# Optimization experiments

Measured on AMD Instinct MI355X. Metric: run time of the kernel, lower is better.

The kernel has to match this reference:

```python
import jax, jax.numpy as jnp
import numpy as np

B, T, D = 2, 4096, 768
H = 12
HD = D // H  # 64
SCALE = 1.0 / np.sqrt(HD)


def setup_inputs() -> dict:
    key = jax.random.key(0)
    k1, k2, k3 = jax.random.split(key, 3)
    x = jax.random.normal(k1, (B, T, D), dtype=jnp.float32)
    W_qkv = jax.random.normal(k2, (D, 3 * D), dtype=jnp.float32) * (1.0 / np.sqrt(D))
    b_qkv = jnp.zeros((3 * D,), dtype=jnp.float32)
    W_out = jax.random.normal(k3, (D, D), dtype=jnp.float32) * (1.0 / np.sqrt(D))
    b_out = jnp.zeros((D,), dtype=jnp.float32)
    return {"x": x, "W_qkv": W_qkv, "b_qkv": b_qkv, "W_out": W_out, "b_out": b_out}


def reference(x, W_qkv, b_qkv, W_out, b_out):
    Bx, Tx, C = x.shape
    qkv = x @ W_qkv + b_qkv                                  # [B,T,3D]
    qkv = qkv.reshape(Bx, Tx, 3, H, HD).transpose(2, 0, 3, 1, 4)  # [3,B,H,T,hd]
    q, k, v = qkv[0], qkv[1], qkv[2]
    scores = jnp.einsum('bhqd,bhkd->bhqk', q, k) * SCALE      # [B,H,T,T]
    causal = jnp.tril(jnp.ones((Tx, Tx), dtype=bool))
    scores = jnp.where(causal[None, None], scores, -jnp.inf)
    attn = jax.nn.softmax(scores, axis=-1)
    out = jnp.einsum('bhqk,bhkd->bhqd', attn, v)              # [B,H,T,hd]
    out = out.transpose(0, 2, 1, 3).reshape(Bx, Tx, C)        # [B,T,D]
    return out @ W_out + b_out
```

## Files before the change

kernel.cpp:

```cpp
#include <hip/hip_runtime.h>
#include <cstdint>
#include <cstddef>

typedef _Float16 f16x8 __attribute__((ext_vector_type(8)));
typedef _Float16 f16x4 __attribute__((ext_vector_type(4)));
typedef _Float16 f16x2 __attribute__((ext_vector_type(2)));
typedef float    f32x4 __attribute__((ext_vector_type(4)));

#define AS_GLOBAL __attribute__((address_space(1)))
#define AS_LDS    __attribute__((address_space(3)))

__device__ __forceinline__ void load16_to_lds(const _Float16* g, _Float16* l) {
    __builtin_amdgcn_global_load_lds((const AS_GLOBAL void*)g, (AS_LDS void*)l, 16, 0, 0);
}

#define BB   2
#define TT   4096
#define DD   768
#define NH   12
#define HDIM 64
#define D3   2304
#define SC2  (0.125f * 1.44269504088896f)

__global__ __launch_bounds__(256) void prep(const float* __restrict__ x,
                                            _Float16* __restrict__ Xh,
                                            const float* __restrict__ Wqkv,
                                            _Float16* __restrict__ Wqkvt,
                                            const float* __restrict__ Wout,
                                            _Float16* __restrict__ Wot) {
    const int bid = blockIdx.x, tid = threadIdx.x;
    if (bid < 6144) {
        const int i = bid * 1024 + tid * 4;
        float4 v = *(const float4*)(x + i);
        f16x4 h;
        h[0] = (_Float16)v.x; h[1] = (_Float16)v.y;
        h[2] = (_Float16)v.z; h[3] = (_Float16)v.w;
        *(f16x4*)(Xh + i) = h;
        return;
    }
    __shared__ float tile[32][33];
    const float* in; _Float16* out; int C, bx, by;
    if (bid < 7872) {
        const int t = bid - 6144;
        in = Wqkv; out = Wqkvt; C = 2304;
        bx = (t % 72) * 32; by = (t / 72) * 32;
    } else {
        const int t = bid - 7872;
        in = Wout; out = Wot; C = 768;
        bx = (t % 24) * 32; by = (t / 24) * 32;
    }
    const int R = 768;
    const int tx = tid & 31, ty = tid >> 5;
#pragma unroll
    for (int j = 0; j < 32; j += 8)
        tile[ty + j][tx] = in[(size_t)(by + ty + j) * C + bx + tx];
    __syncthreads();
#pragma unroll
    for (int j = 0; j < 32; j += 8)
        out[(size_t)(bx + ty + j) * R + by + tx] = (_Float16)tile[tx][ty + j];
}

template <typename OutT>
__device__ __forceinline__ void gemm_body(const _Float16* __restrict__ A,
                                          const _Float16* __restrict__ Bt,
                                          const float* __restrict__ bias, bool bias_row,
                                          OutT* __restrict__ C, int N, int K,
                                          int m0, int n0,
                                          _Float16* As, _Float16* Bs) {
    const int tid  = threadIdx.x;
    const int wave = tid >> 6, lane = tid & 63, quad = lane >> 4, l16 = lane & 15;
    const int wm = (wave & 1) * 64, wn = (wave >> 1) * 64;
    const int rowc = lane >> 3, part = lane & 7;

    f32x4 acc[4][4];
#pragma unroll
    for (int i = 0; i < 4; ++i)
#pragma unroll
        for (int n = 0; n < 4; ++n) acc[i][n] = f32x4{0.f, 0.f, 0.f, 0.f};

    for (int k0 = 0; k0 < K; k0 += 64) {
        __syncthreads();
#pragma unroll
        for (int cc = 0; cc < 4; ++cc) {
            const int ch = wave * 4 + cc;
            load16_to_lds(A  + (size_t)(m0 + ch * 8 + rowc) * K + k0 + part * 8,
                          As + ch * 512);
            load16_to_lds(Bt + (size_t)(n0 + ch * 8 + rowc) * K + k0 + part * 8,
                          Bs + ch * 512);
        }
        __syncthreads();
#pragma unroll
        for (int i = 0; i < 4; ++i) {
            f16x8 a0 = *(const f16x8*)(As + (wm + i * 16 + l16) * 64 + quad * 8);
            f16x8 a1 = *(const f16x8*)(As + (wm + i * 16 + l16) * 64 + 32 + quad * 8);
#pragma unroll
            for (int n = 0; n < 4; ++n) {
                f16x8 b0 = *(const f16x8*)(Bs + (wn + n * 16 + l16) * 64 + quad * 8);
                f16x8 b1 = *(const f16x8*)(Bs + (wn + n * 16 + l16) * 64 + 32 + quad * 8);
                acc[i][n] = __builtin_amdgcn_mfma_f32_16x16x32_f16(a0, b0, acc[i][n], 0, 0, 0);
                acc[i][n] = __builtin_amdgcn_mfma_f32_16x16x32_f16(a1, b1, acc[i][n], 0, 0, 0);
            }
        }
    }
#pragma unroll
    for (int i = 0; i < 4; ++i)
#pragma unroll
        for (int n = 0; n < 4; ++n)
#pragma unroll
            for (int r = 0; r < 4; ++r) {
                const int row = m0 + wm + i * 16 + quad * 4 + r;
                const int col = n0 + wn + n * 16 + l16;
                const float bv = bias_row ? bias[row] : bias[col];
                C[(size_t)row * N + col] = (OutT)(acc[i][n][r] + bv);
            }
}

__global__ __launch_bounds__(256) void gemm_qkv(const _Float16* __restrict__ Xh,
                                                const _Float16* __restrict__ Wqkvt,
                                                const float* __restrict__ bqkv,
                                                _Float16* __restrict__ QKh,
                                                _Float16* __restrict__ VtG) {
    __shared__ __align__(16) _Float16 As[128 * 64];
    __shared__ __align__(16) _Float16 Bs[128 * 64];
    const int bid = blockIdx.x;
    if (bid < 768) {
        const int bx = bid % 12, by = bid / 12;
        gemm_body<_Float16>(Xh, Wqkvt, bqkv, false, QKh, 1536, DD,
                            by * 128, bx * 128, As, Bs);
    } else {
        const int t = bid - 768;
        const int bx = t % 64, by = t / 64;
        gemm_body<_Float16>(Wqkvt + (size_t)1536 * DD, Xh, bqkv + 1536, true, VtG,
                            8192, DD, by * 128, bx * 128, As, Bs);
    }
}

__global__ __launch_bounds__(256) void gemm_out(const _Float16* __restrict__ A,
                                                const _Float16* __restrict__ Bt,
                                                const float* __restrict__ bias,
                                                float* __restrict__ C) {
    __shared__ __align__(16) _Float16 As[128 * 64];
    __shared__ __align__(16) _Float16 Bs[128 * 64];
    gemm_body<float>(A, Bt, bias, false, C, DD, DD,
                     (int)blockIdx.y * 128, (int)blockIdx.x * 128, As, Bs);
}

__global__ __launch_bounds__(256) void attn_kernel(const _Float16* __restrict__ qk,
                                                   const _Float16* __restrict__ vt,
                                                   _Float16* __restrict__ ao) {
    __shared__ __align__(16) _Float16 Ks[2][64 * 64];
    __shared__ __align__(16) _Float16 Vs[2][64 * 64];
    __shared__ __align__(16) _Float16 Ps[4][32 * 32];

    const int L    = blockIdx.x;
    const int xcd  = L & 7;
    const int r_   = L >> 3;
    const int gIdx = r_ % 3;
    const int qt   = 63 - r_ / 3;
    const int g    = gIdx * 8 + xcd;
    const int b = g / NH, h = g % NH;

    const int tid = threadIdx.x;
    const int wave = tid >> 6, lane = tid & 63, quad = lane >> 4, l16 = lane & 15;
    const int wq = wave >> 1, wk = wave & 1;

    f16x8 ones;
#pragma unroll
    for (int j = 0; j < 8; ++j) ones[j] = (_Float16)1.0f;

    int vK[2], vV[2];
#pragma unroll
    for (int p = 0; p < 2; ++p) {
        const int j   = wave * 16 + p * 8 + (lane >> 3);
        const int sig = (j >> 5) * 32 + (j & 15) * 2 + ((j >> 4) & 1);
        const int cdk = (lane & 7) ^ (j & 7);
        vK[p] = (b * TT + sig) * 1536 + DD + h * HDIM + cdk * 8;
        vV[p] = (h * HDIM + j) * 8192 + b * TT + cdk * 8;
    }
    auto stageK = [&](int buf, int k0) {
        const int kK = k0 * 1536;
#pragma unroll
        for (int p = 0; p < 2; ++p)
            load16_to_lds(qk + (vK[p] + kK), Ks[buf] + (wave * 16 + p * 8) * 64);
    };
    auto stageV = [&](int buf, int k0) {
#pragma unroll
        for (int p = 0; p < 2; ++p)
            load16_to_lds(vt + (vV[p] + k0), Vs[buf] + (wave * 16 + p * 8) * 64);
    };

    _Float16* const PsW = &Ps[wave][0];
    _Float16* pw[2][4];
#pragma unroll
    for (int mq = 0; mq < 2; ++mq)
#pragma unroll
        for (int r = 0; r < 4; ++r) {
            const int row = mq * 16 + quad * 4 + r;
            pw[mq][r] = PsW + row * 32 + (((l16 >> 2) ^ ((row >> 2) & 3)) * 8) + (l16 & 3) * 2;
        }
    const _Float16* pr[2];
#pragma unroll
    for (int mq = 0; mq < 2; ++mq) {
        const int row = mq * 16 + l16;
        pr[mq] = PsW + row * 32 + ((quad ^ ((row >> 2) & 3)) * 8);
    }

    const int q0 = qt * 64;
    const int nkt = qt + 1;
    const int qrow0 = q0 + wq * 32;
    f16x8 aq[2][2];
#pragma unroll
    for (int mq = 0; mq < 2; ++mq) {
        const int qoff = (b * TT + qrow0 + mq * 16 + l16) * 1536 + h * HDIM + quad * 8;
        const _Float16 sc = (_Float16)SC2;
        aq[mq][0] = *(const f16x8*)(qk + qoff) * sc;
        aq[mq][1] = *(const f16x8*)(qk + qoff + 32) * sc;
    }
    f32x4 o[2][4], lac[2];
#pragma unroll
    for (int mq = 0; mq < 2; ++mq) {
#pragma unroll
        for (int n = 0; n < 4; ++n) o[mq][n] = f32x4{0.f, 0.f, 0.f, 0.f};
        lac[mq] = f32x4{0.f, 0.f, 0.f, 0.f};
    }

    const int posv = (wk * 4 + quad) ^ (l16 & 7);

    auto pv = [&](int vbuf) {
        f16x8 ap0 = *(const f16x8*)pr[0];
        f16x8 ap1 = *(const f16x8*)pr[1];
        lac[0] = __builtin_amdgcn_mfma_f32_16x16x32_f16(ap0, ones, lac[0], 0, 0, 0);
        lac[1] = __builtin_amdgcn_mfma_f32_16x16x32_f16(ap1, ones, lac[1], 0, 0, 0);
#pragma unroll
        for (int n = 0; n < 4; ++n) {
            f16x8 bv = *(const f16x8*)(Vs[vbuf] + (n * 16 + l16) * 64 + posv * 8);
            o[0][n] = __builtin_amdgcn_mfma_f32_16x16x32_f16(ap0, bv, o[0][n], 0, 0, 0);
            o[1][n] = __builtin_amdgcn_mfma_f32_16x16x32_f16(ap1, bv, o[1][n], 0, 0, 0);
        }
    };

    stageK(0, 0);
    int cur = 0;
    for (int kt = 0; kt < nkt; ++kt) {
        __syncthreads();
        if (kt + 1 < nkt) stageK(cur ^ 1, (kt + 1) * 64);
        stageV(cur, kt * 64);

        __builtin_amdgcn_s_setprio(1);
        f32x4 s[2][2];
#pragma unroll
        for (int mq = 0; mq < 2; ++mq)
#pragma unroll
            for (int n1 = 0; n1 < 2; ++n1) s[mq][n1] = f32x4{0.f, 0.f, 0.f, 0.f};
#pragma unroll
        for (int kh = 0; kh < 2; ++kh)
#pragma unroll
            for (int n1 = 0; n1 < 2; ++n1) {
                const int rowK = (wk * 2 + n1) * 16 + l16;
                const int pos = (kh * 4 + quad) ^ (l16 & 7);
                f16x8 bk = *(const f16x8*)(Ks[cur] + rowK * 64 + pos * 8);
                s[0][n1] = __builtin_amdgcn_mfma_f32_16x16x32_f16(aq[0][kh], bk, s[0][n1], 0, 0, 0);
                s[1][n1] = __builtin_amdgcn_mfma_f32_16x16x32_f16(aq[1][kh], bk, s[1][n1], 0, 0, 0);
            }

        if (kt > 0) pv(cur ^ 1);
        __builtin_amdgcn_s_setprio(0);

        if (kt == nkt - 1) {
#pragma unroll
            for (int mq = 0; mq < 2; ++mq) {
                const int qr = qrow0 + mq * 16 + quad * 4;
#pragma unroll
                for (int n1 = 0; n1 < 2; ++n1) {
                    const int kg = kt * 64 + wk * 32 + l16 * 2 + n1;
#pragma unroll
                    for (int r = 0; r < 4; ++r)
                        if (kg > qr + r) s[mq][n1][r] = -1e30f;
                }
            }
        }

#pragma unroll
        for (int mq = 0; mq < 2; ++mq)
#pragma unroll
            for (int r = 0; r < 4; ++r) {
                f16x2 pk;
                pk[0] = (_Float16)__builtin_amdgcn_exp2f(s[mq][0][r]);
                pk[1] = (_Float16)__builtin_amdgcn_exp2f(s[mq][1][r]);
                *(f16x2*)pw[mq][r] = pk;
            }
        cur ^= 1;
    }

    __syncthreads();
    pv(cur ^ 1);

    __syncthreads();
    float* const Ksf = (float*)&Ks[0][0];
    float* const Psf = (float*)&Ps[0][0];
    if (wk) {
#pragma unroll
        for (int mq = 0; mq < 2; ++mq) {
            if (l16 == 0)
                *(f32x4*)(Psf + wq * 32 + mq * 16 + quad * 4) = lac[mq];
#pragma unroll
            for (int n = 0; n < 4; ++n)
                *(f32x4*)(Ksf + wq * 2048 + (mq * 4 + n) * 256 + lane * 4) = o[mq][n];
        }
    }
    __syncthreads();
    if (!wk) {
#pragma unroll
        for (int mq = 0; mq < 2; ++mq) {
            f32x4 lp = *(const f32x4*)(Psf + wq * 32 + mq * 16 + quad * 4);
            f32x4 inv;
#pragma unroll
            for (int r = 0; r < 4; ++r) inv[r] = 1.0f / (lac[mq][r] + lp[r]);
#pragma unroll
            for (int n = 0; n < 4; ++n) {
                f32x4 op = *(const f32x4*)(Ksf + wq * 2048 + (mq * 4 + n) * 256 + lane * 4);
#pragma unroll
                for (int r = 0; r < 4; ++r) {
                    const int ooff = (b * TT + qrow0 + mq * 16 + quad * 4 + r) * DD + h * HDIM + l16;
                    ao[ooff + n * 16] = (_Float16)((o[mq][n][r] + op[r]) * inv[r]);
                }
            }
        }
    }
}

extern "C" void kernel_launch(void* const* d_in, const int* in_sizes, int n_in,
                              void* d_out, int out_size, void* d_ws, size_t ws_size,
                              hipStream_t stream) {
    const float* x     = (const float*)d_in[0];
    const float* Wqkv  = (const float*)d_in[1];
    const float* bqkv  = (const float*)d_in[2];
    const float* Wout  = (const float*)d_in[3];
    const float* bout  = (const float*)d_in[4];
    float* out = (float*)d_out;

    char* ws = (char*)d_ws;
    _Float16* Xh    = (_Float16*)ws;  ws += (size_t)BB * TT * DD * 2;
    _Float16* Wqkvt = (_Float16*)ws;  ws += (size_t)D3 * DD * 2;
    _Float16* Wot   = (_Float16*)ws;  ws += (size_t)DD * DD * 2;
    _Float16* QKh   = (_Float16*)ws;  ws += (size_t)BB * TT * 1536 * 2;
    _Float16* VtG   = (_Float16*)ws;  ws += (size_t)DD * BB * TT * 2;
    _Float16* AOh   = (_Float16*)ws;  ws += (size_t)BB * TT * DD * 2;

    prep<<<8448, 256, 0, stream>>>(x, Xh, Wqkv, Wqkvt, Wout, Wot);

    gemm_qkv<<<1152, 256, 0, stream>>>(Xh, Wqkvt, bqkv, QKh, VtG);

    attn_kernel<<<1536, 256, 0, stream>>>(QKh, VtG, AOh);

    gemm_out<<<dim3(DD / 128, (BB * TT) / 128), 256, 0, stream>>>(AOh, Wot, bout, out);
}
```

Before: 245.8 us.

## Keep softmax probabilities in registers by transposing QK MFMA, dropping LDS round-trip

```diff
diff --git a/kernel.cpp b/kernel.cpp
--- a/kernel.cpp
+++ b/kernel.cpp
@@ -4,7 +4,6 @@
 
 typedef _Float16 f16x8 __attribute__((ext_vector_type(8)));
 typedef _Float16 f16x4 __attribute__((ext_vector_type(4)));
-typedef _Float16 f16x2 __attribute__((ext_vector_type(2)));
 typedef float    f32x4 __attribute__((ext_vector_type(4)));
 
 #define AS_GLOBAL __attribute__((address_space(1)))
@@ -145,12 +144,11 @@
                      (int)blockIdx.y * 128, (int)blockIdx.x * 128, As, Bs);
 }
 
-__global__ __launch_bounds__(256) void attn_kernel(const _Float16* __restrict__ qk,
-                                                   const _Float16* __restrict__ vt,
-                                                   _Float16* __restrict__ ao) {
+__global__ __launch_bounds__(256, 5) void attn_kernel(const _Float16* __restrict__ qk,
+                                                      const _Float16* __restrict__ vt,
+                                                      _Float16* __restrict__ ao) {
     __shared__ __align__(16) _Float16 Ks[2][64 * 64];
     __shared__ __align__(16) _Float16 Vs[2][64 * 64];
-    __shared__ __align__(16) _Float16 Ps[4][32 * 32];
 
     const int L    = blockIdx.x;
     const int xcd  = L & 7;
@@ -164,50 +162,31 @@
     const int wave = tid >> 6, lane = tid & 63, quad = lane >> 4, l16 = lane & 15;
     const int wq = wave >> 1, wk = wave & 1;
 
-    f16x8 ones;
-#pragma unroll
-    for (int j = 0; j < 8; ++j) ones[j] = (_Float16)1.0f;
+    f16x4 ones4;
+#pragma unroll
+    for (int j = 0; j < 4; ++j) ones4[j] = (_Float16)1.0f;
 
     int vK[2], vV[2];
 #pragma unroll
     for (int p = 0; p < 2; ++p) {
         const int j   = wave * 16 + p * 8 + (lane >> 3);
-        const int sig = (j >> 5) * 32 + (j & 15) * 2 + ((j >> 4) & 1);
         const int cdk = (lane & 7) ^ (j & 7);
-        vK[p] = (b * TT + sig) * 1536 + DD + h * HDIM + cdk * 8;
+        vK[p] = (b * TT + j) * 1536 + DD + h * HDIM + cdk * 8;
         vV[p] = (h * HDIM + j) * 8192 + b * TT + cdk * 8;
     }
-    auto stageK = [&](int buf, int k0) {
+    auto stage = [&](int buf, int k0) {
         const int kK = k0 * 1536;
 #pragma unroll
-        for (int p = 0; p < 2; ++p)
+        for (int p = 0; p < 2; ++p) {
             load16_to_lds(qk + (vK[p] + kK), Ks[buf] + (wave * 16 + p * 8) * 64);
+            load16_to_lds(vt + (vV[p] + k0), Vs[buf] + (wave * 16 + p * 8) * 64);
+        }
     };
-    auto stageV = [&](int buf, int k0) {
-#pragma unroll
-        for (int p = 0; p < 2; ++p)
-            load16_to_lds(vt + (vV[p] + k0), Vs[buf] + (wave * 16 + p * 8) * 64);
-    };
-
-    _Float16* const PsW = &Ps[wave][0];
-    _Float16* pw[2][4];
-#pragma unroll
-    for (int mq = 0; mq < 2; ++mq)
-#pragma unroll
-        for (int r = 0; r < 4; ++r) {
-            const int row = mq * 16 + quad * 4 + r;
-            pw[mq][r] = PsW + row * 32 + (((l16 >> 2) ^ ((row >> 2) & 3)) * 8) + (l16 & 3) * 2;
-        }
-    const _Float16* pr[2];
-#pragma unroll
-    for (int mq = 0; mq < 2; ++mq) {
-        const int row = mq * 16 + l16;
-        pr[mq] = PsW + row * 32 + ((quad ^ ((row >> 2) & 3)) * 8);
-    }
 
     const int q0 = qt * 64;
     const int nkt = qt + 1;
     const int qrow0 = q0 + wq * 32;
+    const int qr_lane = qrow0 + l16;
     f16x8 aq[2][2];
 #pragma unroll
     for (int mq = 0; mq < 2; ++mq) {
@@ -224,27 +203,11 @@
         lac[mq] = f32x4{0.f, 0.f, 0.f, 0.f};
     }
 
-    const int posv = (wk * 4 + quad) ^ (l16 & 7);
-
-    auto pv = [&](int vbuf) {
-        f16x8 ap0 = *(const f16x8*)pr[0];
-        f16x8 ap1 = *(const f16x8*)pr[1];
-        lac[0] = __builtin_amdgcn_mfma_f32_16x16x32_f16(ap0, ones, lac[0], 0, 0, 0);
-        lac[1] = __builtin_amdgcn_mfma_f32_16x16x32_f16(ap1, ones, lac[1], 0, 0, 0);
-#pragma unroll
-        for (int n = 0; n < 4; ++n) {
-            f16x8 bv = *(const f16x8*)(Vs[vbuf] + (n * 16 + l16) * 64 + posv * 8);
-            o[0][n] = __builtin_amdgcn_mfma_f32_16x16x32_f16(ap0, bv, o[0][n], 0, 0, 0);
-            o[1][n] = __builtin_amdgcn_mfma_f32_16x16x32_f16(ap1, bv, o[1][n], 0, 0, 0);
-        }
-    };
-
-    stageK(0, 0);
+    stage(0, 0);
     int cur = 0;
     for (int kt = 0; kt < nkt; ++kt) {
         __syncthreads();
-        if (kt + 1 < nkt) stageK(cur ^ 1, (kt + 1) * 64);
-        stageV(cur, kt * 64);
+        if (kt + 1 < nkt) stage(cur ^ 1, (kt + 1) * 64);
 
         __builtin_amdgcn_s_setprio(1);
         f32x4 s[2][2];
@@ -259,50 +222,63 @@
                 const int rowK = (wk * 2 + n1) * 16 + l16;
                 const int pos = (kh * 4 + quad) ^ (l16 & 7);
                 f16x8 bk = *(const f16x8*)(Ks[cur] + rowK * 64 + pos * 8);
-                s[0][n1] = __builtin_amdgcn_mfma_f32_16x16x32_f16(aq[0][kh], bk, s[0][n1], 0, 0, 0);
-                s[1][n1] = __builtin_amdgcn_mfma_f32_16x16x32_f16(aq[1][kh], bk, s[1][n1], 0, 0, 0);
-            }
-
-        if (kt > 0) pv(cur ^ 1);
+                s[0][n1] = __builtin_amdgcn_mfma_f32_16x16x32_f16(bk, aq[0][kh], s[0][n1], 0, 0, 0);
+                s[1][n1] = __builtin_amdgcn_mfma_f32_16x16x32_f16(bk, aq[1][kh], s[1][n1], 0, 0, 0);
+            }
         __builtin_amdgcn_s_setprio(0);
 
         if (kt == nkt - 1) {
 #pragma unroll
             for (int mq = 0; mq < 2; ++mq) {
-                const int qr = qrow0 + mq * 16 + quad * 4;
+                const int qr = qr_lane + mq * 16;
 #pragma unroll
                 for (int n1 = 0; n1 < 2; ++n1) {
-                    const int kg = kt * 64 + wk * 32 + l16 * 2 + n1;
+                    const int kg0 = kt * 64 + wk * 32 + n1 * 16 + quad * 4;
 #pragma unroll
                     for (int r = 0; r < 4; ++r)
-                        if (kg > qr + r) s[mq][n1][r] = -1e30f;
+                        if (kg0 + r > qr) s[mq][n1][r] = -1e30f;
                 }
             }
         }
 
+        f16x4 pa[2][2];
 #pragma unroll
         for (int mq = 0; mq < 2; ++mq)
 #pragma unroll
-            for (int r = 0; r < 4; ++r) {
-                f16x2 pk;
-                pk[0] = (_Float16)__builtin_amdgcn_exp2f(s[mq][0][r]);
-                pk[1] = (_Float16)__builtin_amdgcn_exp2f(s[mq][1][r]);
-                *(f16x2*)pw[mq][r] = pk;
-            }
+            for (int n1 = 0; n1 < 2; ++n1)
+#pragma unroll
+                for (int r = 0; r < 4; ++r)
+                    pa[mq][n1][r] = (_Float16)__builtin_amdgcn_exp2f(s[mq][n1][r]);
+
+        __builtin_amdgcn_s_setprio(1);
+#pragma unroll
+        for (int mq = 0; mq < 2; ++mq) {
+            lac[mq] = __builtin_amdgcn_mfma_f32_16x16x16f16(pa[mq][0], ones4, lac[mq], 0, 0, 0);
+            lac[mq] = __builtin_amdgcn_mfma_f32_16x16x16f16(pa[mq][1], ones4, lac[mq], 0, 0, 0);
+        }
+#pragma unroll
+        for (int n1 = 0; n1 < 2; ++n1)
+#pragma unroll
+            for (int n = 0; n < 4; ++n) {
+                const int rowV = n * 16 + l16;
+                const int lc  = wk * 4 + n1 * 2 + (quad >> 1);
+                const int pc  = lc ^ (l16 & 7);
+                f16x4 bv = *(const f16x4*)(Vs[cur] + rowV * 64 + pc * 8 + (quad & 1) * 4);
+                o[0][n] = __builtin_amdgcn_mfma_f32_16x16x16f16(pa[0][n1], bv, o[0][n], 0, 0, 0);
+                o[1][n] = __builtin_amdgcn_mfma_f32_16x16x16f16(pa[1][n1], bv, o[1][n], 0, 0, 0);
+            }
+        __builtin_amdgcn_s_setprio(0);
         cur ^= 1;
     }
-
-    __syncthreads();
-    pv(cur ^ 1);
 
     __syncthreads();
     float* const Ksf = (float*)&Ks[0][0];
-    float* const Psf = (float*)&Ps[0][0];
+    float* const Vsf = (float*)&Vs[0][0];
     if (wk) {
 #pragma unroll
         for (int mq = 0; mq < 2; ++mq) {
             if (l16 == 0)
-                *(f32x4*)(Psf + wq * 32 + mq * 16 + quad * 4) = lac[mq];
+                *(f32x4*)(Vsf + wq * 32 + mq * 16 + quad * 4) = lac[mq];
 #pragma unroll
             for (int n = 0; n < 4; ++n)
                 *(f32x4*)(Ksf + wq * 2048 + (mq * 4 + n) * 256 + lane * 4) = o[mq][n];
@@ -312,7 +288,7 @@
     if (!wk) {
 #pragma unroll
         for (int mq = 0; mq < 2; ++mq) {
-            f32x4 lp = *(const f32x4*)(Psf + wq * 32 + mq * 16 + quad * 4);
+            f32x4 lp = *(const f32x4*)(Vsf + wq * 32 + mq * 16 + quad * 4);
             f32x4 inv;
 #pragma unroll
             for (int r = 0; r < 4; ++r) inv[r] = 1.0f / (lac[mq][r] + lp[r]);
```

Result: no change. 241.2 us (-1.9%).
